# Kernel optimization log

Measured on AMD Instinct MI355X. Metric: run time of the kernel, lower is better.

The kernel has to match this reference:

```python
import jax, jax.numpy as jnp
import numpy as np

B, N, E, D, P = 128, 50000, 300000, 256, 8


def setup_inputs() -> dict:
    key = jax.random.key(0)
    ks = jax.random.split(key, 13)
    scale = 1.0 / np.sqrt(D)  # keep uniform-init logits numerically sane
    return {
        "instruction_batch": jax.random.normal(ks[0], (B, D), jnp.float32),
        "distribution": jax.random.uniform(ks[1], (N,), jnp.float32),
        "node_prop_similarities": jax.random.uniform(ks[2], (B, P), jnp.float32),
        "relation_similarity": jax.random.uniform(ks[3], (B,), jnp.float32),
        "node_attrs": jax.random.normal(ks[4], (N, D), jnp.float32),
        "edge_attrs": jax.random.normal(ks[5], (E, D), jnp.float32),
        "W_node_props": jax.random.uniform(ks[6], (P, D, D), jnp.float32) * scale,
        "W_edge": jax.random.uniform(ks[7], (D, D), jnp.float32) * scale,
        "w_node_score": jax.random.uniform(ks[8], (D,), jnp.float32) * scale,
        "w_rel_score": jax.random.uniform(ks[9], (D,), jnp.float32) * scale,
        "node_indices": jnp.sort(jax.random.randint(ks[10], (N,), 0, B)),
        "edge_batch_indices": jax.random.randint(ks[11], (E,), 0, B),
        "edge_indices": jax.random.randint(ks[12], (2, E), 0, N),
    }


def _segment_softmax(logits, seg, num_segments):
    # softmax over all entries sharing the same segment (= per-graph softmax)
    m = jax.ops.segment_max(logits, seg, num_segments=num_segments)
    e = jnp.exp(logits - m[seg])
    s = jax.ops.segment_sum(e, seg, num_segments=num_segments)
    return e / s[seg]


def reference(instruction_batch, distribution, node_prop_similarities,
              relation_similarity, node_attrs, edge_attrs,
              W_node_props, W_edge, w_node_score, w_rel_score,
              node_indices, edge_batch_indices, edge_indices):
    num_graphs = instruction_batch.shape[0]

    # node_scores[n,d] = elu( sum_p sim[n,p] * instr[n,d] * (W_p @ attr_n)[d] )
    sim_n = node_prop_similarities[node_indices]          # [N, P]
    instr_n = instruction_batch[node_indices]             # [N, D]
    wa = jnp.einsum("pde,ne->npd", W_node_props, node_attrs)  # [N, P, D]
    node_scores = jax.nn.elu(
        jnp.einsum("np,nd,npd->nd", sim_n, instr_n, wa))   # [N, D]

    # edge_scores[e,d] = elu( instr[batch(e),d] * (W_edge @ edge_attr_e)[d] )
    edge_scores = jax.nn.elu(
        instruction_batch[edge_batch_indices] * (edge_attrs @ W_edge.T))  # [E, D]

    # per-graph (sparse) softmax over node state logits
    state_logits = node_scores @ w_node_score              # [N]
    next_states = _segment_softmax(state_logits, node_indices, num_graphs)

    # scatter: aggregate weighted edge messages at destination nodes
    src, dst = edge_indices[0], edge_indices[1]
    msgs = distribution[src, None] * edge_scores           # [E, D]
    agg = jnp.zeros_like(node_scores).at[dst].add(msgs)    # [N, D]
    rel_logits = agg @ w_rel_score                         # [N]
    next_relations = _segment_softmax(rel_logits, node_indices, num_graphs)

    r = relation_similarity[node_indices]                  # [N]
    return r * next_relations + (1.0 - r) * next_states
```

## Files before the change

kernel.cpp:

```cpp
#include <hip/hip_runtime.h>

#define NB 128
#define NN 50000
#define NE 300000
#define ND 256
#define NP 8

typedef __attribute__((ext_vector_type(4))) float f32x4;
typedef __attribute__((ext_vector_type(8))) short s16x8;

__device__ __forceinline__ unsigned short bf16rtn(float f) {
    unsigned int u = __float_as_uint(f);
    unsigned int r = (u + 0x7fffu + ((u >> 16) & 1u)) >> 16;
    return (unsigned short)r;
}

__device__ __forceinline__ int cvtpk(float lo, float hi) {
    int r;
    asm("v_cvt_pk_bf16_f32 %0, %1, %2" : "=v"(r) : "v"(lo), "v"(hi));
    return r;
}

__device__ __forceinline__ s16x8 pack8(f32x4 a, f32x4 b) {
    union { int d[4]; s16x8 v; } u;
    u.d[0] = cvtpk(a[0], a[1]);
    u.d[1] = cvtpk(a[2], a[3]);
    u.d[2] = cvtpk(b[0], b[1]);
    u.d[3] = cvtpk(b[2], b[3]);
    return u.v;
}

__device__ __forceinline__ float eluf(float x) {
    return x > 0.f ? x : __expf(x) - 1.f;
}

__device__ __forceinline__ float rowsum16(float x) {
    int t;
    t = __builtin_amdgcn_update_dpp(0, __float_as_int(x), 0x121, 0xf, 0xf, true);
    x += __int_as_float(t);
    t = __builtin_amdgcn_update_dpp(0, __float_as_int(x), 0x122, 0xf, 0xf, true);
    x += __int_as_float(t);
    t = __builtin_amdgcn_update_dpp(0, __float_as_int(x), 0x124, 0xf, 0xf, true);
    x += __int_as_float(t);
    t = __builtin_amdgcn_update_dpp(0, __float_as_int(x), 0x128, 0xf, 0xf, true);
    x += __int_as_float(t);
    return x;
}

__device__ __forceinline__ void stage_W(char* Wl, const unsigned short* Wsrc,
                                        int tid, int nthr) {
    for (int i = tid; i < 8192; i += nthr) {
        int cg = i >> 9;
        int kk = (i >> 6) & 7;
        int ln = i & 63;
        const unsigned short* src =
            Wsrc + (size_t)(cg * 16 + (ln & 15)) * ND + kk * 32 + (ln >> 4) * 8;
        *(s16x8*)(Wl + i * 16) = *(const s16x8*)src;
    }
}

__global__ void k_starts(const int* __restrict__ idx, int* __restrict__ starts,
                         float* __restrict__ rel_logits,
                         const int* __restrict__ eidx,
                         const float* __restrict__ dist,
                         float* __restrict__ dscg) {
    int n = blockIdx.x * blockDim.x + threadIdx.x;
    if (n < NE) dscg[n] = dist[eidx[n]];
    if (n >= NN) return;
    rel_logits[n] = 0.f;
    int cur = idx[n];
    int prev = (n == 0) ? -1 : idx[n - 1];
    for (int b2 = prev + 1; b2 <= cur; ++b2) starts[b2] = n;
    if (n == NN - 1)
        for (int b2 = cur + 1; b2 <= NB; ++b2) starts[b2] = NN;
}

__global__ void k_wedge_bf16(const float* __restrict__ w, unsigned short* __restrict__ o) {
    int i = (blockIdx.x * 256 + threadIdx.x) * 4;
    f32x4 v = *(const f32x4*)(w + i);
    o[i + 0] = bf16rtn(v[0]); o[i + 1] = bf16rtn(v[1]);
    o[i + 2] = bf16rtn(v[2]); o[i + 3] = bf16rtn(v[3]);
}

__global__ __launch_bounds__(256) void k_weff(
    const float* __restrict__ sim, const float* __restrict__ Wp,
    unsigned short* __restrict__ Weff)
{
    int chunk = blockIdx.x * 256 + threadIdx.x;
    int off = chunk * 8;
    float wp[NP][8];
#pragma unroll
    for (int p = 0; p < NP; ++p) {
        const float* src = Wp + (size_t)p * ND * ND + off;
        f32x4 w0 = *(const f32x4*)src;
        f32x4 w1 = *(const f32x4*)(src + 4);
        wp[p][0] = w0[0]; wp[p][1] = w0[1]; wp[p][2] = w0[2]; wp[p][3] = w0[3];
        wp[p][4] = w1[0]; wp[p][5] = w1[1]; wp[p][6] = w1[2]; wp[p][7] = w1[3];
    }
    int b0 = blockIdx.y * 16;
    for (int bb = 0; bb < 16; ++bb) {
        int b = b0 + bb;
        float g[8] = {0.f, 0.f, 0.f, 0.f, 0.f, 0.f, 0.f, 0.f};
#pragma unroll
        for (int p = 0; p < NP; ++p) {
            float s = sim[b * NP + p];
#pragma unroll
            for (int j = 0; j < 8; ++j) g[j] += s * wp[p][j];
        }
        s16x8 v;
#pragma unroll
        for (int j = 0; j < 8; ++j) v[j] = (short)bf16rtn(g[j]);
        *(s16x8*)(Weff + (size_t)b * ND * ND + off) = v;
    }
}

__global__ __launch_bounds__(1024, 4) void k_edges(
    const float* __restrict__ instr, const float* __restrict__ dscg,
    const float* __restrict__ eattrs, const unsigned short* __restrict__ Wbf,
    const float* __restrict__ wrs, const int* __restrict__ ebidx,
    const int* __restrict__ eidx, float* __restrict__ rel_logits)
{
    __shared__ char Wl[131072];

    int tid = threadIdx.x;
    int lane = tid & 63;
    int wave = tid >> 6;
    int l15 = lane & 15;
    int q = lane >> 4;

    stage_W(Wl, Wbf, tid, 1024);
    __syncthreads();

    int gw = blockIdx.x * 16 + wave;
    const int NT = NE / 16;
    for (int t = gw; t < NT; t += 4096) {
        int e0 = t * 16;
        int e4 = e0 + 4 * q;
        int eb0 = ebidx[e4 + 0], eb1 = ebidx[e4 + 1];
        int eb2 = ebidx[e4 + 2], eb3 = ebidx[e4 + 3];
        float dv0 = dscg[e4 + 0], dv1 = dscg[e4 + 1];
        float dv2 = dscg[e4 + 2], dv3 = dscg[e4 + 3];
        int dd0 = eidx[NE + e4 + 0], dd1 = eidx[NE + e4 + 1];
        int dd2 = eidx[NE + e4 + 2], dd3 = eidx[NE + e4 + 3];

        const float* ib0 = instr + (size_t)eb0 * ND + l15;
        const float* ib1 = instr + (size_t)eb1 * ND + l15;
        const float* ib2 = instr + (size_t)eb2 * ND + l15;
        const float* ib3 = instr + (size_t)eb3 * ND + l15;

        const float* arow = eattrs + (size_t)(e0 + l15) * ND + q * 8;
        s16x8 afr[8];
#pragma unroll
        for (int kk = 0; kk < 8; ++kk) {
            f32x4 a0 = *(const f32x4*)(arow + kk * 32);
            f32x4 a1 = *(const f32x4*)(arow + kk * 32 + 4);
            afr[kk] = pack8(a0, a1);
        }

        float nv0 = ib0[0], nv1 = ib1[0], nv2 = ib2[0], nv3 = ib3[0];
        float nw = wrs[l15];

        float p0 = 0.f, p1 = 0.f, p2 = 0.f, p3 = 0.f;
#pragma unroll 1
        for (int cg = 0; cg < 16; ++cg) {
            float v0 = nv0, v1 = nv1, v2 = nv2, v3 = nv3, wvc = nw;
            int cn = (cg + 1 < 16 ? cg + 1 : 15) * 16;
            nv0 = ib0[cn]; nv1 = ib1[cn]; nv2 = ib2[cn]; nv3 = ib3[cn];
            nw = wrs[cn + l15];

            f32x4 acc = {0.f, 0.f, 0.f, 0.f};
            const char* fb = Wl + cg * 8192 + lane * 16;
#pragma unroll
            for (int kk = 0; kk < 8; ++kk) {
                s16x8 bf = *(const s16x8*)(fb + kk * 1024);
                acc = __builtin_amdgcn_mfma_f32_16x16x32_bf16(afr[kk], bf, acc, 0, 0, 0);
            }
            p0 += wvc * eluf(v0 * acc[0]);
            p1 += wvc * eluf(v1 * acc[1]);
            p2 += wvc * eluf(v2 * acc[2]);
            p3 += wvc * eluf(v3 * acc[3]);
        }
        p0 = rowsum16(p0); p1 = rowsum16(p1);
        p2 = rowsum16(p2); p3 = rowsum16(p3);
        if (l15 == 0) {
            atomicAdd(&rel_logits[dd0], dv0 * p0);
            atomicAdd(&rel_logits[dd1], dv1 * p1);
            atomicAdd(&rel_logits[dd2], dv2 * p2);
            atomicAdd(&rel_logits[dd3], dv3 * p3);
        }
    }
}

__global__ __launch_bounds__(1024, 4) void k_nodes(
    const float* __restrict__ instr, const unsigned short* __restrict__ Weff,
    const float* __restrict__ attrs, const float* __restrict__ wns,
    const int* __restrict__ starts, float* __restrict__ state_logits)
{
    __shared__ char Wl[131072];

    int b = blockIdx.x >> 1;
    int half = blockIdx.x & 1;
    int s0 = starts[b], s1 = starts[b + 1];
    int nt = (s1 - s0 + 15) >> 4;

    int tid = threadIdx.x;
    int lane = tid & 63;
    int wave = tid >> 6;
    int l15 = lane & 15;
    int q = lane >> 4;

    stage_W(Wl, Weff + (size_t)b * ND * ND, tid, 1024);
    __syncthreads();

    const float* irow = instr + (size_t)b * ND + l15;
    for (int t = half * 16 + wave; t < nt; t += 32) {
        int n0 = s0 + t * 16;
        int arn = n0 + l15;
        bool valid = arn < s1;
        const float* arow = attrs + (size_t)arn * ND + q * 8;
        s16x8 afr[8];
#pragma unroll
        for (int kk = 0; kk < 8; ++kk) {
            f32x4 a0 = {0.f, 0.f, 0.f, 0.f}, a1 = {0.f, 0.f, 0.f, 0.f};
            if (valid) {
                a0 = *(const f32x4*)(arow + kk * 32);
                a1 = *(const f32x4*)(arow + kk * 32 + 4);
            }
            afr[kk] = pack8(a0, a1);
        }

        float p0 = 0.f, p1 = 0.f, p2 = 0.f, p3 = 0.f;
#pragma unroll 1
        for (int cg = 0; cg < 16; ++cg) {
            f32x4 acc = {0.f, 0.f, 0.f, 0.f};
            const char* fb = Wl + cg * 8192 + lane * 16;
#pragma unroll
            for (int kk = 0; kk < 8; ++kk) {
                s16x8 bf = *(const s16x8*)(fb + kk * 1024);
                acc = __builtin_amdgcn_mfma_f32_16x16x32_bf16(afr[kk], bf, acc, 0, 0, 0);
            }
            int c = cg * 16;
            float ivc = irow[c];
            float wvc = wns[c + l15];
            p0 += wvc * eluf(ivc * acc[0]);
            p1 += wvc * eluf(ivc * acc[1]);
            p2 += wvc * eluf(ivc * acc[2]);
            p3 += wvc * eluf(ivc * acc[3]);
        }
        p0 = rowsum16(p0); p1 = rowsum16(p1);
        p2 = rowsum16(p2); p3 = rowsum16(p3);
        if (l15 == 0) {
            int n = n0 + 4 * q;
            if (n + 0 < s1) state_logits[n + 0] = p0;
            if (n + 1 < s1) state_logits[n + 1] = p1;
            if (n + 2 < s1) state_logits[n + 2] = p2;
            if (n + 3 < s1) state_logits[n + 3] = p3;
        }
    }
}

__global__ __launch_bounds__(256) void k_softmax_mix(
    const float* __restrict__ state_l, const float* __restrict__ rel_l,
    const int* __restrict__ starts, const float* __restrict__ relsim,
    float* __restrict__ out)
{
    __shared__ float wms[4], wmr[4], wss[4], wsr[4];
    int b = blockIdx.x;
    int s0 = starts[b], s1 = starts[b + 1];
    if (s1 <= s0) return;
    int tid = threadIdx.x, lane = tid & 63, wave = tid >> 6;

    float ms = -3.4e38f, mr = -3.4e38f;
    for (int n = s0 + tid; n < s1; n += 256) {
        ms = fmaxf(ms, state_l[n]);
        mr = fmaxf(mr, rel_l[n]);
    }
#pragma unroll
    for (int m = 1; m < 64; m <<= 1) {
        ms = fmaxf(ms, __shfl_xor(ms, m, 64));
        mr = fmaxf(mr, __shfl_xor(mr, m, 64));
    }
    if (lane == 0) { wms[wave] = ms; wmr[wave] = mr; }
    __syncthreads();
    ms = fmaxf(fmaxf(wms[0], wms[1]), fmaxf(wms[2], wms[3]));
    mr = fmaxf(fmaxf(wmr[0], wmr[1]), fmaxf(wmr[2], wmr[3]));

    float ss = 0.f, sr = 0.f;
    for (int n = s0 + tid; n < s1; n += 256) {
        ss += __expf(state_l[n] - ms);
        sr += __expf(rel_l[n] - mr);
    }
#pragma unroll
    for (int m = 1; m < 64; m <<= 1) {
        ss += __shfl_xor(ss, m, 64);
        sr += __shfl_xor(sr, m, 64);
    }
    if (lane == 0) { wss[wave] = ss; wsr[wave] = sr; }
    __syncthreads();
    ss = wss[0] + wss[1] + wss[2] + wss[3];
    sr = wsr[0] + wsr[1] + wsr[2] + wsr[3];

    float rb = relsim[b];
    float iss = 1.f / ss, isr = 1.f / sr;
    for (int n = s0 + tid; n < s1; n += 256) {
        out[n] = rb * __expf(rel_l[n] - mr) * isr
               + (1.f - rb) * __expf(state_l[n] - ms) * iss;
    }
}

extern "C" void kernel_launch(void* const* d_in, const int* in_sizes, int n_in,
                              void* d_out, int out_size, void* d_ws, size_t ws_size,
                              hipStream_t stream) {
    const float* instr  = (const float*)d_in[0];
    const float* dist   = (const float*)d_in[1];
    const float* sim    = (const float*)d_in[2];
    const float* relsim = (const float*)d_in[3];
    const float* nattr  = (const float*)d_in[4];
    const float* eattr  = (const float*)d_in[5];
    const float* Wp     = (const float*)d_in[6];
    const float* We     = (const float*)d_in[7];
    const float* wns    = (const float*)d_in[8];
    const float* wrs    = (const float*)d_in[9];
    const int* nidx     = (const int*)d_in[10];
    const int* ebidx    = (const int*)d_in[11];
    const int* eidx     = (const int*)d_in[12];
    float* out = (float*)d_out;

    char* ws = (char*)d_ws;
    float* rel_logits   = (float*)ws;
    float* state_logits = rel_logits + NN;
    int* starts         = (int*)(ws + 400000);
    unsigned short* Wbf = (unsigned short*)(ws + 400640);
    unsigned short* Weff= (unsigned short*)(ws + 532480);
    float* dscg         = (float*)(ws + 17309696);

    k_wedge_bf16<<<64, 256, 0, stream>>>(We, Wbf);
    k_weff<<<dim3(32, 8), 256, 0, stream>>>(sim, Wp, Weff);
    k_starts<<<(NE + 255) / 256, 256, 0, stream>>>(nidx, starts, rel_logits,
                                                   eidx, dist, dscg);
    k_edges<<<256, 1024, 0, stream>>>(instr, dscg, eattr, Wbf, wrs,
                                      ebidx, eidx, rel_logits);
    k_nodes<<<256, 1024, 0, stream>>>(instr, Weff, nattr, wns, starts,
                                      state_logits);
    k_softmax_mix<<<NB, 256, 0, stream>>>(state_logits, rel_logits, starts,
                                          relsim, out);
}
```

Baseline: 152.4 us.

## Merge prep kernels and co-schedule edge and node GEMMs in one launch

Folds the three small prep kernels (W_edge bf16 cast, per-graph Weff build, starts/dscg setup) into one launch, and merges the edge and node MFMA kernels into a single 512-block grid whose blocks branch on blockIdx. This removes launch gaps and lets the memory-bound edge work overlap the node work across CUs. It also swaps the edge wave-to-tile mapping so neighbouring blocks take adjacent tiles, and raises wave priority around the MFMA loops with s_setprio. The cost is a heterogeneous grid, where uneven block durations can cause tail imbalance.

```diff
diff --git a/kernel.cpp b/kernel.cpp
--- a/kernel.cpp
+++ b/kernel.cpp
@@ -59,66 +59,71 @@
     }
 }
 
-__global__ void k_starts(const int* __restrict__ idx, int* __restrict__ starts,
-                         float* __restrict__ rel_logits,
-                         const int* __restrict__ eidx,
-                         const float* __restrict__ dist,
-                         float* __restrict__ dscg) {
-    int n = blockIdx.x * blockDim.x + threadIdx.x;
-    if (n < NE) dscg[n] = dist[eidx[n]];
-    if (n >= NN) return;
-    rel_logits[n] = 0.f;
-    int cur = idx[n];
-    int prev = (n == 0) ? -1 : idx[n - 1];
-    for (int b2 = prev + 1; b2 <= cur; ++b2) starts[b2] = n;
-    if (n == NN - 1)
-        for (int b2 = cur + 1; b2 <= NB; ++b2) starts[b2] = NN;
-}
-
-__global__ void k_wedge_bf16(const float* __restrict__ w, unsigned short* __restrict__ o) {
-    int i = (blockIdx.x * 256 + threadIdx.x) * 4;
-    f32x4 v = *(const f32x4*)(w + i);
-    o[i + 0] = bf16rtn(v[0]); o[i + 1] = bf16rtn(v[1]);
-    o[i + 2] = bf16rtn(v[2]); o[i + 3] = bf16rtn(v[3]);
-}
-
-__global__ __launch_bounds__(256) void k_weff(
+__global__ __launch_bounds__(256) void k_prep(
+    const float* __restrict__ We, unsigned short* __restrict__ Wbf,
     const float* __restrict__ sim, const float* __restrict__ Wp,
-    unsigned short* __restrict__ Weff)
+    unsigned short* __restrict__ Weff,
+    const int* __restrict__ nidx, int* __restrict__ starts,
+    float* __restrict__ rel_logits,
+    const int* __restrict__ eidx, const float* __restrict__ dist,
+    float* __restrict__ dscg)
 {
-    int chunk = blockIdx.x * 256 + threadIdx.x;
-    int off = chunk * 8;
-    float wp[NP][8];
-#pragma unroll
-    for (int p = 0; p < NP; ++p) {
-        const float* src = Wp + (size_t)p * ND * ND + off;
-        f32x4 w0 = *(const f32x4*)src;
-        f32x4 w1 = *(const f32x4*)(src + 4);
-        wp[p][0] = w0[0]; wp[p][1] = w0[1]; wp[p][2] = w0[2]; wp[p][3] = w0[3];
-        wp[p][4] = w1[0]; wp[p][5] = w1[1]; wp[p][6] = w1[2]; wp[p][7] = w1[3];
-    }
-    int b0 = blockIdx.y * 16;
-    for (int bb = 0; bb < 16; ++bb) {
-        int b = b0 + bb;
-        float g[8] = {0.f, 0.f, 0.f, 0.f, 0.f, 0.f, 0.f, 0.f};
+    int bid = blockIdx.x;
+    int tid = threadIdx.x;
+    if (bid < 64) {
+        int i = (bid * 256 + tid) * 4;
+        f32x4 v = *(const f32x4*)(We + i);
+        Wbf[i + 0] = bf16rtn(v[0]); Wbf[i + 1] = bf16rtn(v[1]);
+        Wbf[i + 2] = bf16rtn(v[2]); Wbf[i + 3] = bf16rtn(v[3]);
+    } else if (bid < 320) {
+        int wb = bid - 64;
+        int chunk = (wb & 31) * 256 + tid;
+        int off = chunk * 8;
+        float wp[NP][8];
 #pragma unroll
         for (int p = 0; p < NP; ++p) {
-            float s = sim[b * NP + p];
-#pragma unroll
-            for (int j = 0; j < 8; ++j) g[j] += s * wp[p][j];
+            const float* src = Wp + (size_t)p * ND * ND + off;
+            f32x4 w0 = *(const f32x4*)src;
+            f32x4 w1 = *(const f32x4*)(src + 4);
+            wp[p][0] = w0[0]; wp[p][1] = w0[1]; wp[p][2] = w0[2]; wp[p][3] = w0[3];
+            wp[p][4] = w1[0]; wp[p][5] = w1[1]; wp[p][6] = w1[2]; wp[p][7] = w1[3];
         }
-        s16x8 v;
-#pragma unroll
-        for (int j = 0; j < 8; ++j) v[j] = (short)bf16rtn(g[j]);
-        *(s16x8*)(Weff + (size_t)b * ND * ND + off) = v;
-    }
-}
-
-__global__ __launch_bounds__(1024, 4) void k_edges(
+        int b0 = (wb >> 5) * 16;
+        for (int bb = 0; bb < 16; ++bb) {
+            int b = b0 + bb;
+            float g[8] = {0.f, 0.f, 0.f, 0.f, 0.f, 0.f, 0.f, 0.f};
+#pragma unroll
+            for (int p = 0; p < NP; ++p) {
+                float s = sim[b * NP + p];
+#pragma unroll
+                for (int j = 0; j < 8; ++j) g[j] += s * wp[p][j];
+            }
+            s16x8 v;
+#pragma unroll
+            for (int j = 0; j < 8; ++j) v[j] = (short)bf16rtn(g[j]);
+            *(s16x8*)(Weff + (size_t)b * ND * ND + off) = v;
+        }
+    } else {
+        int n = (bid - 320) * 256 + tid;
+        if (n < NE) dscg[n] = dist[eidx[n]];
+        if (n >= NN) return;
+        rel_logits[n] = 0.f;
+        int cur = nidx[n];
+        int prev = (n == 0) ? -1 : nidx[n - 1];
+        for (int b2 = prev + 1; b2 <= cur; ++b2) starts[b2] = n;
+        if (n == NN - 1)
+            for (int b2 = cur + 1; b2 <= NB; ++b2) starts[b2] = NN;
+    }
+}
+
+__global__ __launch_bounds__(1024, 4) void k_main(
     const float* __restrict__ instr, const float* __restrict__ dscg,
     const float* __restrict__ eattrs, const unsigned short* __restrict__ Wbf,
     const float* __restrict__ wrs, const int* __restrict__ ebidx,
-    const int* __restrict__ eidx, float* __restrict__ rel_logits)
+    const int* __restrict__ eidx, float* __restrict__ rel_logits,
+    const unsigned short* __restrict__ Weff, const float* __restrict__ nattrs,
+    const float* __restrict__ wns, const int* __restrict__ starts,
+    float* __restrict__ state_logits)
 {
     __shared__ char Wl[131072];
 
@@ -128,133 +133,126 @@
     int l15 = lane & 15;
     int q = lane >> 4;
 
-    stage_W(Wl, Wbf, tid, 1024);
-    __syncthreads();
-
-    int gw = blockIdx.x * 16 + wave;
-    const int NT = NE / 16;
-    for (int t = gw; t < NT; t += 4096) {
-        int e0 = t * 16;
-        int e4 = e0 + 4 * q;
-        int eb0 = ebidx[e4 + 0], eb1 = ebidx[e4 + 1];
-        int eb2 = ebidx[e4 + 2], eb3 = ebidx[e4 + 3];
-        float dv0 = dscg[e4 + 0], dv1 = dscg[e4 + 1];
-        float dv2 = dscg[e4 + 2], dv3 = dscg[e4 + 3];
-        int dd0 = eidx[NE + e4 + 0], dd1 = eidx[NE + e4 + 1];
-        int dd2 = eidx[NE + e4 + 2], dd3 = eidx[NE + e4 + 3];
-
-        const float* ib0 = instr + (size_t)eb0 * ND + l15;
-        const float* ib1 = instr + (size_t)eb1 * ND + l15;
-        const float* ib2 = instr + (size_t)eb2 * ND + l15;
-        const float* ib3 = instr + (size_t)eb3 * ND + l15;
-
-        const float* arow = eattrs + (size_t)(e0 + l15) * ND + q * 8;
-        s16x8 afr[8];
-#pragma unroll
-        for (int kk = 0; kk < 8; ++kk) {
-            f32x4 a0 = *(const f32x4*)(arow + kk * 32);
-            f32x4 a1 = *(const f32x4*)(arow + kk * 32 + 4);
-            afr[kk] = pack8(a0, a1);
+    if (blockIdx.x < 256) {
+        stage_W(Wl, Wbf, tid, 1024);
+        __syncthreads();
+
+        int gw = wave * 256 + blockIdx.x;
+        const int NT = NE / 16;
+        for (int t = gw; t < NT; t += 4096) {
+            int e0 = t * 16;
+            int e4 = e0 + 4 * q;
+            int eb0 = ebidx[e4 + 0], eb1 = ebidx[e4 + 1];
+            int eb2 = ebidx[e4 + 2], eb3 = ebidx[e4 + 3];
+            float dv0 = dscg[e4 + 0], dv1 = dscg[e4 + 1];
+            float dv2 = dscg[e4 + 2], dv3 = dscg[e4 + 3];
+            int dd0 = eidx[NE + e4 + 0], dd1 = eidx[NE + e4 + 1];
+            int dd2 = eidx[NE + e4 + 2], dd3 = eidx[NE + e4 + 3];
+
+            const float* ib0 = instr + (size_t)eb0 * ND + l15;
+            const float* ib1 = instr + (size_t)eb1 * ND + l15;
+            const float* ib2 = instr + (size_t)eb2 * ND + l15;
+            const float* ib3 = instr + (size_t)eb3 * ND + l15;
+
+            const float* arow = eattrs + (size_t)(e0 + l15) * ND + q * 8;
+            s16x8 afr[8];
+#pragma unroll
+            for (int kk = 0; kk < 8; ++kk) {
+                f32x4 a0 = *(const f32x4*)(arow + kk * 32);
+                f32x4 a1 = *(const f32x4*)(arow + kk * 32 + 4);
+                afr[kk] = pack8(a0, a1);
+            }
+
+            float nv0 = ib0[0], nv1 = ib1[0], nv2 = ib2[0], nv3 = ib3[0];
+            float nw = wrs[l15];
+
+            float p0 = 0.f, p1 = 0.f, p2 = 0.f, p3 = 0.f;
+#pragma unroll 1
+            for (int cg = 0; cg < 16; ++cg) {
+                float v0 = nv0, v1 = nv1, v2 = nv2, v3 = nv3, wvc = nw;
+                int cn = (cg + 1 < 16 ? cg + 1 : 15) * 16;
+                nv0 = ib0[cn]; nv1 = ib1[cn]; nv2 = ib2[cn]; nv3 = ib3[cn];
+                nw = wrs[cn + l15];
+
+                f32x4 acc = {0.f, 0.f, 0.f, 0.f};
+                const char* fb = Wl + cg * 8192 + lane * 16;
+                __builtin_amdgcn_s_setprio(1);
+#pragma unroll
+                for (int kk = 0; kk < 8; ++kk) {
+                    s16x8 bf = *(const s16x8*)(fb + kk * 1024);
+                    acc = __builtin_amdgcn_mfma_f32_16x16x32_bf16(afr[kk], bf, acc, 0, 0, 0);
+                }
+                __builtin_amdgcn_s_setprio(0);
+                p0 += wvc * eluf(v0 * acc[0]);
+                p1 += wvc * eluf(v1 * acc[1]);
+                p2 += wvc * eluf(v2 * acc[2]);
+                p3 += wvc * eluf(v3 * acc[3]);
+            }
+            p0 = rowsum16(p0); p1 = rowsum16(p1);
+            p2 = rowsum16(p2); p3 = rowsum16(p3);
+            if (l15 == 0) {
+                atomicAdd(&rel_logits[dd0], dv0 * p0);
+                atomicAdd(&rel_logits[dd1], dv1 * p1);
+                atomicAdd(&rel_logits[dd2], dv2 * p2);
+                atomicAdd(&rel_logits[dd3], dv3 * p3);
+            }
         }
-
-        float nv0 = ib0[0], nv1 = ib1[0], nv2 = ib2[0], nv3 = ib3[0];
-        float nw = wrs[l15];
-
-        float p0 = 0.f, p1 = 0.f, p2 = 0.f, p3 = 0.f;
+    } else {
+        int nb = blockIdx.x - 256;
+        int b = nb >> 1;
+        int half = nb & 1;
+        int s0 = starts[b], s1 = starts[b + 1];
+        int nt = (s1 - s0 + 15) >> 4;
+
+        stage_W(Wl, Weff + (size_t)b * ND * ND, tid, 1024);
+        __syncthreads();
+
+        const float* irow = instr + (size_t)b * ND + l15;
+        for (int t = half * 16 + wave; t < nt; t += 32) {
+            int n0 = s0 + t * 16;
+            int arn = n0 + l15;
+            bool valid = arn < s1;
+            const float* arow = nattrs + (size_t)arn * ND + q * 8;
+            s16x8 afr[8];
+#pragma unroll
+            for (int kk = 0; kk < 8; ++kk) {
+                f32x4 a0 = {0.f, 0.f, 0.f, 0.f}, a1 = {0.f, 0.f, 0.f, 0.f};
+                if (valid) {
+                    a0 = *(const f32x4*)(arow + kk * 32);
+                    a1 = *(const f32x4*)(arow + kk * 32 + 4);
+                }
+                afr[kk] = pack8(a0, a1);
+            }
+
+            float p0 = 0.f, p1 = 0.f, p2 = 0.f, p3 = 0.f;
 #pragma unroll 1
-        for (int cg = 0; cg < 16; ++cg) {
-            float v0 = nv0, v1 = nv1, v2 = nv2, v3 = nv3, wvc = nw;
-            int cn = (cg + 1 < 16 ? cg + 1 : 15) * 16;
-            nv0 = ib0[cn]; nv1 = ib1[cn]; nv2 = ib2[cn]; nv3 = ib3[cn];
-            nw = wrs[cn + l15];
-
-            f32x4 acc = {0.f, 0.f, 0.f, 0.f};
-            const char* fb = Wl + cg * 8192 + lane * 16;
-#pragma unroll
-            for (int kk = 0; kk < 8; ++kk) {
-                s16x8 bf = *(const s16x8*)(fb + kk * 1024);
-                acc = __builtin_amdgcn_mfma_f32_16x16x32_bf16(afr[kk], bf, acc, 0, 0, 0);
-            }
-            p0 += wvc * eluf(v0 * acc[0]);
-            p1 += wvc * eluf(v1 * acc[1]);
-            p2 += wvc * eluf(v2 * acc[2]);
-            p3 += wvc * eluf(v3 * acc[3]);
-        }
-        p0 = rowsum16(p0); p1 = rowsum16(p1);
-        p2 = rowsum16(p2); p3 = rowsum16(p3);
-        if (l15 == 0) {
-            atomicAdd(&rel_logits[dd0], dv0 * p0);
-            atomicAdd(&rel_logits[dd1], dv1 * p1);
-            atomicAdd(&rel_logits[dd2], dv2 * p2);
-            atomicAdd(&rel_logits[dd3], dv3 * p3);
-        }
-    }
-}
-
-__global__ __launch_bounds__(1024, 4) void k_nodes(
-    const float* __restrict__ instr, const unsigned short* __restrict__ Weff,
-    const float* __restrict__ attrs, const float* __restrict__ wns,
-    const int* __restrict__ starts, float* __restrict__ state_logits)
-{
-    __shared__ char Wl[131072];
-
-    int b = blockIdx.x >> 1;
-    int half = blockIdx.x & 1;
-    int s0 = starts[b], s1 = starts[b + 1];
-    int nt = (s1 - s0 + 15) >> 4;
-
-    int tid = threadIdx.x;
-    int lane = tid & 63;
-    int wave = tid >> 6;
-    int l15 = lane & 15;
-    int q = lane >> 4;
-
-    stage_W(Wl, Weff + (size_t)b * ND * ND, tid, 1024);
-    __syncthreads();
-
-    const float* irow = instr + (size_t)b * ND + l15;
-    for (int t = half * 16 + wave; t < nt; t += 32) {
-        int n0 = s0 + t * 16;
-        int arn = n0 + l15;
-        bool valid = arn < s1;
-        const float* arow = attrs + (size_t)arn * ND + q * 8;
-        s16x8 afr[8];
-#pragma unroll
-        for (int kk = 0; kk < 8; ++kk) {
-            f32x4 a0 = {0.f, 0.f, 0.f, 0.f}, a1 = {0.f, 0.f, 0.f, 0.f};
-            if (valid) {
-                a0 = *(const f32x4*)(arow + kk * 32);
-                a1 = *(const f32x4*)(arow + kk * 32 + 4);
-            }
-            afr[kk] = pack8(a0, a1);
-        }
-
-        float p0 = 0.f, p1 = 0.f, p2 = 0.f, p3 = 0.f;
-#pragma unroll 1
-        for (int cg = 0; cg < 16; ++cg) {
-            f32x4 acc = {0.f, 0.f, 0.f, 0.f};
-            const char* fb = Wl + cg * 8192 + lane * 16;
-#pragma unroll
-            for (int kk = 0; kk < 8; ++kk) {
-                s16x8 bf = *(const s16x8*)(fb + kk * 1024);
-                acc = __builtin_amdgcn_mfma_f32_16x16x32_bf16(afr[kk], bf, acc, 0, 0, 0);
-            }
-            int c = cg * 16;
-            float ivc = irow[c];
-            float wvc = wns[c + l15];
-            p0 += wvc * eluf(ivc * acc[0]);
-            p1 += wvc * eluf(ivc * acc[1]);
-            p2 += wvc * eluf(ivc * acc[2]);
-            p3 += wvc * eluf(ivc * acc[3]);
-        }
-        p0 = rowsum16(p0); p1 = rowsum16(p1);
-        p2 = rowsum16(p2); p3 = rowsum16(p3);
-        if (l15 == 0) {
-            int n = n0 + 4 * q;
-            if (n + 0 < s1) state_logits[n + 0] = p0;
-            if (n + 1 < s1) state_logits[n + 1] = p1;
-            if (n + 2 < s1) state_logits[n + 2] = p2;
-            if (n + 3 < s1) state_logits[n + 3] = p3;
+            for (int cg = 0; cg < 16; ++cg) {
+                f32x4 acc = {0.f, 0.f, 0.f, 0.f};
+                const char* fb = Wl + cg * 8192 + lane * 16;
+                __builtin_amdgcn_s_setprio(1);
+#pragma unroll
+                for (int kk = 0; kk < 8; ++kk) {
+                    s16x8 bf = *(const s16x8*)(fb + kk * 1024);
+                    acc = __builtin_amdgcn_mfma_f32_16x16x32_bf16(afr[kk], bf, acc, 0, 0, 0);
+                }
+                __builtin_amdgcn_s_setprio(0);
+                int c = cg * 16;
+                float ivc = irow[c];
+                float wvc = wns[c + l15];
+                p0 += wvc * eluf(ivc * acc[0]);
+                p1 += wvc * eluf(ivc * acc[1]);
+                p2 += wvc * eluf(ivc * acc[2]);
+                p3 += wvc * eluf(ivc * acc[3]);
+            }
+            p0 = rowsum16(p0); p1 = rowsum16(p1);
+            p2 = rowsum16(p2); p3 = rowsum16(p3);
+            if (l15 == 0) {
+                int n = n0 + 4 * q;
+                if (n + 0 < s1) state_logits[n + 0] = p0;
+                if (n + 1 < s1) state_logits[n + 1] = p1;
+                if (n + 2 < s1) state_logits[n + 2] = p2;
+                if (n + 3 < s1) state_logits[n + 3] = p3;
+            }
         }
     }
 }
@@ -334,14 +332,11 @@
     unsigned short* Weff= (unsigned short*)(ws + 532480);
     float* dscg         = (float*)(ws + 17309696);
 
-    k_wedge_bf16<<<64, 256, 0, stream>>>(We, Wbf);
-    k_weff<<<dim3(32, 8), 256, 0, stream>>>(sim, Wp, Weff);
-    k_starts<<<(NE + 255) / 256, 256, 0, stream>>>(nidx, starts, rel_logits,
-                                                   eidx, dist, dscg);
-    k_edges<<<256, 1024, 0, stream>>>(instr, dscg, eattr, Wbf, wrs,
-                                      ebidx, eidx, rel_logits);
-    k_nodes<<<256, 1024, 0, stream>>>(instr, Weff, nattr, wns, starts,
-                                      state_logits);
+    k_prep<<<320 + (NE + 255) / 256, 256, 0, stream>>>(
+        We, Wbf, sim, Wp, Weff, nidx, starts, rel_logits, eidx, dist, dscg);
+    k_main<<<512, 1024, 0, stream>>>(instr, dscg, eattr, Wbf, wrs, ebidx, eidx,
+                                     rel_logits, Weff, nattr, wns, starts,
+                                     state_logits);
     k_softmax_mix<<<NB, 256, 0, stream>>>(state_logits, rel_logits, starts,
                                           relsim, out);
 }
```

After: 129.1 us (median of 2 runs). -15.3%, faster.
